# Performance work log

Measured on AMD Instinct MI355X. Metric: run time of the kernel, lower is better.

Reference implementation:

```python
import jax, jax.numpy as jnp
import numpy as np

N = 20000
N_RET = 20000
NEG_SLOPE = 0.2


def _xavier(key, shape):
    fan_in, fan_out = shape[-2], shape[-1]
    limit = float(np.sqrt(6.0 / (fan_in + fan_out)))
    return jax.random.uniform(key, shape, jnp.float32, -limit, limit)


def setup_inputs() -> dict:
    key = jax.random.key(0)
    ks = jax.random.split(key, 24)
    E = 320000
    inp = {
        "emb_u": jax.random.normal(ks[0], (N, 256), jnp.float32),
        "emb_t": jax.random.normal(ks[1], (N, 256), jnp.float32),
        "src_u": jax.random.randint(ks[2], (E,), 0, N, jnp.int32),
        "trg_u": jax.random.randint(ks[3], (E,), 0, N, jnp.int32),
        "src_t": jax.random.randint(ks[4], (E,), 0, N, jnp.int32),
        "trg_t": jax.random.randint(ks[5], (E,), 0, N, jnp.int32),
    }
    # SpGATLayer params per stack (u=user graph, t=tweet graph), 2 layers each.
    # layer0: f_in=256, layer1: f_in = 64*4 = 256 (concat of heads); f_out=64, H=4.
    i = 6
    for side in ("u", "t"):
        for l in range(2):
            inp[f"w_{side}{l}"] = _xavier(ks[i], (4, 256, 64)); i += 1
            inp[f"a_src_{side}{l}"] = _xavier(ks[i], (4, 64, 1))[:, :, 0]; i += 1
            inp[f"a_trg_{side}{l}"] = _xavier(ks[i], (4, 64, 1))[:, :, 0]; i += 1
    inp["fc_w"] = _xavier(ks[i], (128, 16)); i += 1  # [in_features, out_features]
    inp["fc_b"] = jnp.zeros((16,), jnp.float32)
    return inp


def gat_layer(h, w, a_src, a_trg, src, trg):
    # h: [n, f_in], w: [H, f_in, F], a_*: [H, F]
    hp = jnp.einsum("nf,hfo->hno", h, w)                 # [H, n, F]
    attn_src = jnp.einsum("hno,ho->nh", hp, a_src)        # [n, H]
    attn_trg = jnp.einsum("hno,ho->nh", hp, a_trg)        # [n, H]
    e = jax.nn.leaky_relu(attn_src[src] + attn_trg[trg], NEG_SLOPE)  # [E, H]
    exp_e = jnp.exp(e - jnp.max(e))
    denom = jax.ops.segment_sum(exp_e, trg, num_segments=N)[trg] + 1e-16
    attn = (exp_e / denom)[:, :, None]                    # [E, H, 1]
    hp_lift = jnp.transpose(hp, (1, 0, 2))[src]           # [E, H, F]
    return jax.ops.segment_sum(hp_lift * attn, trg, num_segments=N)  # [n, H, F]


def run_stack(h, src, trg, w0, as0, at0, w1, as1, at1):
    x = gat_layer(h, w0, as0, at0, src, trg)
    x = jax.nn.elu(x.reshape(N, -1))                      # [n, H*F]
    x = gat_layer(x, w1, as1, at1, src, trg)
    return x.mean(axis=1)                                 # [n, F]


def reference(emb_u, emb_t, src_u, trg_u, src_t, trg_t,
              w_u0, a_src_u0, a_trg_u0, w_u1, a_src_u1, a_trg_u1,
              w_t0, a_src_t0, a_trg_t0, w_t1, a_src_t1, a_trg_t1,
              fc_w, fc_b):
    out_u = run_stack(emb_u, src_u, trg_u, w_u0, a_src_u0, a_trg_u0, w_u1, a_src_u1, a_trg_u1)
    out_t = run_stack(emb_t, src_t, trg_t, w_t0, a_src_t0, a_trg_t0, w_t1, a_src_t1, a_trg_t1)
    ret = jnp.concatenate([out_u[:N_RET], out_t[:N_RET]], axis=-1)   # [n_ret, 128]
    logits = ret @ fc_w + fc_b                                       # [n_ret, 16]
    return jax.nn.log_softmax(logits, axis=-1)
```

## Files before the change

kernel.cpp:

```cpp
#include <hip/hip_runtime.h>
#include <hip/hip_bf16.h>

#define NEG_SLOPE 0.2f

typedef unsigned short u16;
typedef u16 u16x8 __attribute__((ext_vector_type(8)));
typedef u16 u16x4 __attribute__((ext_vector_type(4)));
typedef short s16x8 __attribute__((ext_vector_type(8)));
typedef float f32x4 __attribute__((ext_vector_type(4)));

__device__ __forceinline__ u16 f2bf(float x) {
    unsigned u = __float_as_uint(x);
    return (u16)((u + 0x7fffu + ((u >> 16) & 1u)) >> 16);
}
__device__ __forceinline__ float bf2f(u16 h) {
    return __uint_as_float(((unsigned)h) << 16);
}

__global__ __launch_bounds__(256) void splitx_k(const float* __restrict__ X,
                                                u16* __restrict__ Xh,
                                                u16* __restrict__ Xl, int total4)
{
    int i = blockIdx.x * 256 + threadIdx.x;
    if (i >= total4) return;
    float4 v = *(const float4*)(X + (size_t)i * 4);
    float f[4] = { v.x, v.y, v.z, v.w };
    u16x4 hi, lo;
    #pragma unroll
    for (int j = 0; j < 4; ++j) {
        u16 h = f2bf(f[j]);
        hi[j] = h;
        lo[j] = f2bf(f[j] - bf2f(h));
    }
    *(u16x4*)(Xh + (size_t)i * 4) = hi;
    *(u16x4*)(Xl + (size_t)i * 4) = lo;
}

__global__ __launch_bounds__(256) void wsplit4_k(
    const float* __restrict__ w0, const float* __restrict__ w1,
    const float* __restrict__ w2, const float* __restrict__ w3,
    u16* __restrict__ Wht, u16* __restrict__ Wlt)
{
    int tid = blockIdx.x * 256 + threadIdx.x;
    int which = tid >> 16;
    int idx = tid & 65535;
    const float* W = (which == 0) ? w0 : (which == 1) ? w1 : (which == 2) ? w2 : w3;
    int f = idx & 63, k = (idx >> 6) & 255, h = idx >> 14;
    float x = W[idx];
    u16 hi = f2bf(x);
    u16 lo = f2bf(x - bf2f(hi));
    int o = (which << 16) + (h * 64 + f) * 256 + k;
    Wht[o] = hi; Wlt[o] = lo;
}

__global__ __launch_bounds__(256) void gemm_mfma_k(
    const u16* __restrict__ Xh, const u16* __restrict__ Xl,
    const u16* __restrict__ Wht, const u16* __restrict__ Wlt,
    const float* __restrict__ a_src, const float* __restrict__ a_trg,
    u16* __restrict__ HPB, float* __restrict__ as_, float* __restrict__ at_,
    int n)
{
    const int row0 = blockIdx.x * 64;
    const int h    = blockIdx.y;
    const int t = threadIdx.x;
    const int l = t & 63;
    const int wc = (t >> 6) & 1;
    const int wr = (t >> 7) & 1;

    __shared__ u16 Ah[64 * 40], Al[64 * 40], Bh[64 * 40], Bl[64 * 40];

    const int sr = t >> 2, sp = t & 3;
    const int arow = (row0 + sr < n) ? (row0 + sr) : (n - 1);
    const u16* gAh = Xh + (size_t)arow * 256 + sp * 8;
    const u16* gAl = Xl + (size_t)arow * 256 + sp * 8;
    const u16* gBh = Wht + (size_t)(h * 64 + sr) * 256 + sp * 8;
    const u16* gBl = Wlt + (size_t)(h * 64 + sr) * 256 + sp * 8;
    const int ldst = sr * 40 + sp * 8;

    const int ra0 = (wr * 32 + (l & 15)) * 40 + (l >> 4) * 8;
    const int ca0 = (wc * 32 + (l & 15)) * 40 + (l >> 4) * 8;

    f32x4 acc00 = {0.f, 0.f, 0.f, 0.f}, acc01 = acc00, acc10 = acc00, acc11 = acc00;

    for (int k0 = 0; k0 < 256; k0 += 32) {
        __syncthreads();
        *(u16x8*)&Ah[ldst] = *(const u16x8*)(gAh + k0);
        *(u16x8*)&Al[ldst] = *(const u16x8*)(gAl + k0);
        *(u16x8*)&Bh[ldst] = *(const u16x8*)(gBh + k0);
        *(u16x8*)&Bl[ldst] = *(const u16x8*)(gBl + k0);
        __syncthreads();

        s16x8 a0h = *(const s16x8*)&Ah[ra0];
        s16x8 a1h = *(const s16x8*)&Ah[ra0 + 640];
        s16x8 a0l = *(const s16x8*)&Al[ra0];
        s16x8 a1l = *(const s16x8*)&Al[ra0 + 640];
        s16x8 b0h = *(const s16x8*)&Bh[ca0];
        s16x8 b1h = *(const s16x8*)&Bh[ca0 + 640];
        s16x8 b0l = *(const s16x8*)&Bl[ca0];
        s16x8 b1l = *(const s16x8*)&Bl[ca0 + 640];

        acc00 = __builtin_amdgcn_mfma_f32_16x16x32_bf16(a0h, b0h, acc00, 0, 0, 0);
        acc01 = __builtin_amdgcn_mfma_f32_16x16x32_bf16(a0h, b1h, acc01, 0, 0, 0);
        acc10 = __builtin_amdgcn_mfma_f32_16x16x32_bf16(a1h, b0h, acc10, 0, 0, 0);
        acc11 = __builtin_amdgcn_mfma_f32_16x16x32_bf16(a1h, b1h, acc11, 0, 0, 0);
        acc00 = __builtin_amdgcn_mfma_f32_16x16x32_bf16(a0h, b0l, acc00, 0, 0, 0);
        acc01 = __builtin_amdgcn_mfma_f32_16x16x32_bf16(a0h, b1l, acc01, 0, 0, 0);
        acc10 = __builtin_amdgcn_mfma_f32_16x16x32_bf16(a1h, b0l, acc10, 0, 0, 0);
        acc11 = __builtin_amdgcn_mfma_f32_16x16x32_bf16(a1h, b1l, acc11, 0, 0, 0);
        acc00 = __builtin_amdgcn_mfma_f32_16x16x32_bf16(a0l, b0h, acc00, 0, 0, 0);
        acc01 = __builtin_amdgcn_mfma_f32_16x16x32_bf16(a0l, b1h, acc01, 0, 0, 0);
        acc10 = __builtin_amdgcn_mfma_f32_16x16x32_bf16(a1l, b0h, acc10, 0, 0, 0);
        acc11 = __builtin_amdgcn_mfma_f32_16x16x32_bf16(a1l, b1h, acc11, 0, 0, 0);
    }

    const int cl = wc * 32 + (l & 15);
    const int rb = row0 + wr * 32 + ((l >> 4) << 2);
    const float pa0 = a_src[h * 64 + cl], pa1 = a_src[h * 64 + cl + 16];
    const float pb0 = a_trg[h * 64 + cl], pb1 = a_trg[h * 64 + cl + 16];

    #pragma unroll
    for (int r = 0; r < 4; ++r) {
        int g0 = rb + r, g1 = rb + 16 + r;
        float s0 = acc00[r] * pa0 + acc01[r] * pa1;
        float t0 = acc00[r] * pb0 + acc01[r] * pb1;
        float s1 = acc10[r] * pa0 + acc11[r] * pa1;
        float t1 = acc10[r] * pb0 + acc11[r] * pb1;
        #pragma unroll
        for (int off = 8; off; off >>= 1) {
            s0 += __shfl_xor(s0, off, 16); t0 += __shfl_xor(t0, off, 16);
            s1 += __shfl_xor(s1, off, 16); t1 += __shfl_xor(t1, off, 16);
        }
        if (g0 < n) {
            HPB[(size_t)g0 * 256 + h * 64 + cl]      = f2bf(acc00[r]);
            HPB[(size_t)g0 * 256 + h * 64 + cl + 16] = f2bf(acc01[r]);
            if ((l & 15) == 0) {
                atomicAdd(&as_[g0 * 4 + h], s0);
                atomicAdd(&at_[g0 * 4 + h], t0);
            }
        }
        if (g1 < n) {
            HPB[(size_t)g1 * 256 + h * 64 + cl]      = f2bf(acc10[r]);
            HPB[(size_t)g1 * 256 + h * 64 + cl + 16] = f2bf(acc11[r]);
            if ((l & 15) == 0) {
                atomicAdd(&as_[g1 * 4 + h], s1);
                atomicAdd(&at_[g1 * 4 + h], t1);
            }
        }
    }
}

__global__ void hist2_k(const int* __restrict__ tu, const int* __restrict__ tt,
                        int* __restrict__ counts, int* __restrict__ ranks,
                        int E, int N)
{
    int e = blockIdx.x * blockDim.x + threadIdx.x;
    if (e < E)          ranks[e] = atomicAdd(&counts[tu[e]], 1);
    else if (e < 2 * E) ranks[e] = atomicAdd(&counts[N + tt[e - E]], 1);
}

__global__ __launch_bounds__(1024) void scan2_k(const int* __restrict__ counts_all,
                                                int* __restrict__ starts_all, int n)
{
    const int T = 1024;
    const int* counts = counts_all + blockIdx.x * n;
    int* starts = starts_all + blockIdx.x * (n + 1);
    int t = threadIdx.x;
    int chunk = (n + T - 1) / T;
    int beg = t * chunk;
    int end = min(beg + chunk, n);
    int sum = 0;
    for (int i = beg; i < end; ++i) sum += counts[i];
    __shared__ int lds[T];
    lds[t] = sum;
    __syncthreads();
    for (int off = 1; off < T; off <<= 1) {
        int v = (t >= off) ? lds[t - off] : 0;
        __syncthreads();
        lds[t] += v;
        __syncthreads();
    }
    int run = lds[t] - sum;
    for (int i = beg; i < end; ++i) { starts[i] = run; run += counts[i]; }
    if (t == T - 1) starts[n] = lds[T - 1];
}

__global__ void scatter2_k(const int* __restrict__ su, const int* __restrict__ st,
                           const int* __restrict__ tu, const int* __restrict__ tt,
                           const int* __restrict__ starts_all,
                           const int* __restrict__ ranks, int* __restrict__ srcs,
                           int E, int N)
{
    int e = blockIdx.x * blockDim.x + threadIdx.x;
    if (e < E) {
        srcs[starts_all[tu[e]] + ranks[e]] = su[e];
    } else if (e < 2 * E) {
        int ee = e - E;
        const int* st1 = starts_all + (N + 1);
        srcs[E + st1[tt[ee]] + ranks[e]] = st[ee];
    }
}

template<int LAYER>
__global__ __launch_bounds__(256) void aggregate_k(
    const u16* __restrict__ HPB, const float* __restrict__ as_,
    const float* __restrict__ at_, const int* __restrict__ starts,
    const int* __restrict__ srcs,
    u16* __restrict__ oh, u16* __restrict__ ol, float* __restrict__ of, int n)
{
    const int w = threadIdx.x >> 6;
    const int l = threadIdx.x & 63;
    const int v = blockIdx.x * 4 + w;
    if (v >= n) return;
    const int h = l >> 4;
    const int s0 = starts[v], s1 = starts[v + 1];
    const float atv = at_[v * 4 + h];
    const size_t lo4 = (size_t)l * 4;

    float4 ac0 = make_float4(0.f, 0.f, 0.f, 0.f), ac1 = ac0, ac2 = ac0, ac3 = ac0;
    float dn0 = 0.f, dn1 = 0.f, dn2 = 0.f, dn3 = 0.f;

    for (int base = s0; base < s1; base += 64) {
        int m = min(64, s1 - base);
        int s_l = (base + l < s1) ? srcs[base + l] : 0;
        int i = 0;
        for (; i + 3 < m; i += 4) {
            int sa = __shfl(s_l, i, 64);
            int sb = __shfl(s_l, i + 1, 64);
            int sc = __shfl(s_l, i + 2, 64);
            int sd = __shfl(s_l, i + 3, 64);
            u16x4 va = *(const u16x4*)(HPB + (size_t)sa * 256 + lo4);
            u16x4 vb = *(const u16x4*)(HPB + (size_t)sb * 256 + lo4);
            u16x4 vc = *(const u16x4*)(HPB + (size_t)sc * 256 + lo4);
            u16x4 vd = *(const u16x4*)(HPB + (size_t)sd * 256 + lo4);
            float ea = as_[sa * 4 + h] + atv;
            float eb = as_[sb * 4 + h] + atv;
            float ec = as_[sc * 4 + h] + atv;
            float ed = as_[sd * 4 + h] + atv;
            ea = (ea > 0.f) ? ea : NEG_SLOPE * ea;
            eb = (eb > 0.f) ? eb : NEG_SLOPE * eb;
            ec = (ec > 0.f) ? ec : NEG_SLOPE * ec;
            ed = (ed > 0.f) ? ed : NEG_SLOPE * ed;
            float pA = expf(ea), pB = expf(eb), pC = expf(ec), pD = expf(ed);
            dn0 += pA; dn1 += pB; dn2 += pC; dn3 += pD;
            ac0.x += pA * bf2f(va[0]); ac0.y += pA * bf2f(va[1]);
            ac0.z += pA * bf2f(va[2]); ac0.w += pA * bf2f(va[3]);
            ac1.x += pB * bf2f(vb[0]); ac1.y += pB * bf2f(vb[1]);
            ac1.z += pB * bf2f(vb[2]); ac1.w += pB * bf2f(vb[3]);
            ac2.x += pC * bf2f(vc[0]); ac2.y += pC * bf2f(vc[1]);
            ac2.z += pC * bf2f(vc[2]); ac2.w += pC * bf2f(vc[3]);
            ac3.x += pD * bf2f(vd[0]); ac3.y += pD * bf2f(vd[1]);
            ac3.z += pD * bf2f(vd[2]); ac3.w += pD * bf2f(vd[3]);
        }
        for (; i < m; ++i) {
            int sa = __shfl(s_l, i, 64);
            u16x4 va = *(const u16x4*)(HPB + (size_t)sa * 256 + lo4);
            float ea = as_[sa * 4 + h] + atv;
            ea = (ea > 0.f) ? ea : NEG_SLOPE * ea;
            float pA = expf(ea);
            dn0 += pA;
            ac0.x += pA * bf2f(va[0]); ac0.y += pA * bf2f(va[1]);
            ac0.z += pA * bf2f(va[2]); ac0.w += pA * bf2f(va[3]);
        }
    }

    float4 acc = make_float4(ac0.x + ac1.x + ac2.x + ac3.x,
                             ac0.y + ac1.y + ac2.y + ac3.y,
                             ac0.z + ac1.z + ac2.z + ac3.z,
                             ac0.w + ac1.w + ac2.w + ac3.w);
    float r = 1.f / (dn0 + dn1 + dn2 + dn3 + 1e-16f);
    acc.x *= r; acc.y *= r; acc.z *= r; acc.w *= r;

    if (LAYER == 0) {
        float f[4] = { acc.x, acc.y, acc.z, acc.w };
        u16x4 hi, lo;
        #pragma unroll
        for (int c = 0; c < 4; ++c) {
            float e = (f[c] > 0.f) ? f[c] : expm1f(f[c]);
            u16 hh = f2bf(e);
            hi[c] = hh;
            lo[c] = f2bf(e - bf2f(hh));
        }
        *(u16x4*)(oh + (size_t)v * 256 + lo4) = hi;
        *(u16x4*)(ol + (size_t)v * 256 + lo4) = lo;
    } else {
        acc.x += __shfl_xor(acc.x, 16, 64); acc.y += __shfl_xor(acc.y, 16, 64);
        acc.z += __shfl_xor(acc.z, 16, 64); acc.w += __shfl_xor(acc.w, 16, 64);
        acc.x += __shfl_xor(acc.x, 32, 64); acc.y += __shfl_xor(acc.y, 32, 64);
        acc.z += __shfl_xor(acc.z, 32, 64); acc.w += __shfl_xor(acc.w, 32, 64);
        if (l < 16) {
            acc.x *= 0.25f; acc.y *= 0.25f; acc.z *= 0.25f; acc.w *= 0.25f;
            *(float4*)(of + (size_t)v * 64 + l * 4) = acc;
        }
    }
}

__global__ __launch_bounds__(256) void final_k(
    const float* __restrict__ out_u, const float* __restrict__ out_t,
    const float* __restrict__ fcw, const float* __restrict__ fcb,
    float* __restrict__ out, int nret)
{
    int gid = blockIdx.x * blockDim.x + threadIdx.x;
    int nn = gid >> 4;
    int j  = gid & 15;
    if (nn >= nret) return;
    const float* ru = out_u + (size_t)nn * 64;
    const float* rt = out_t + (size_t)nn * 64;
    float acc = fcb[j];
    #pragma unroll 8
    for (int k = 0; k < 64; ++k) acc += ru[k] * fcw[k * 16 + j];
    #pragma unroll 8
    for (int k = 0; k < 64; ++k) acc += rt[k] * fcw[(64 + k) * 16 + j];

    float m = acc;
    for (int off = 8; off; off >>= 1) m = fmaxf(m, __shfl_xor(m, off, 16));
    float ex = expf(acc - m);
    float s = ex;
    for (int off = 8; off; off >>= 1) s += __shfl_xor(s, off, 16);
    out[(size_t)nn * 16 + j] = acc - m - logf(s);
}

extern "C" void kernel_launch(void* const* d_in, const int* in_sizes, int n_in,
                              void* d_out, int out_size, void* d_ws, size_t ws_size,
                              hipStream_t stream)
{
    const int N = in_sizes[0] / 256;
    const int E = in_sizes[2];
    const int NRET = out_size / 16;

    const float* emb[2]  = { (const float*)d_in[0], (const float*)d_in[1] };
    const int*   srcI[2] = { (const int*)d_in[2], (const int*)d_in[4] };
    const int*   trgI[2] = { (const int*)d_in[3], (const int*)d_in[5] };
    const float* fcw = (const float*)d_in[18];
    const float* fcb = (const float*)d_in[19];

    char* p = (char*)d_ws;
    u16* hpb = (u16*)p;   p += (size_t)N * 256 * 2;
    u16* xh  = (u16*)p;   p += (size_t)N * 256 * 2;
    u16* xl  = (u16*)p;   p += (size_t)N * 256 * 2;
    u16* wht = (u16*)p;   p += (size_t)4 * 65536 * 2;
    u16* wlt = (u16*)p;   p += (size_t)4 * 65536 * 2;
    float* asat = (float*)p; p += (size_t)N * 32 * 4;
    float* out_s[2];
    out_s[0] = (float*)p; p += (size_t)N * 64 * 4;
    out_s[1] = (float*)p; p += (size_t)N * 64 * 4;
    int* starts2 = (int*)p; p += (size_t)2 * (N + 1) * 4;
    int* counts2 = (int*)p; p += (size_t)2 * N * 4;
    int* ranks2  = (int*)p; p += (size_t)2 * E * 4;
    int* srcs2   = (int*)p; p += (size_t)2 * E * 4;

    const int E2B = (2 * E + 255) / 256;
    const dim3 gemm_grid((N + 63) / 64, 4);
    const int split_blocks = (N * 64 + 255) / 256;
    const int agg_grid = (N + 3) / 4;

    hipMemsetAsync(asat, 0, (size_t)N * 32 * 4, stream);
    hipMemsetAsync(counts2, 0, (size_t)2 * N * 4, stream);

    hist2_k<<<E2B, 256, 0, stream>>>(trgI[0], trgI[1], counts2, ranks2, E, N);
    scan2_k<<<2, 1024, 0, stream>>>(counts2, starts2, N);
    scatter2_k<<<E2B, 256, 0, stream>>>(srcI[0], srcI[1], trgI[0], trgI[1],
                                        starts2, ranks2, srcs2, E, N);

    wsplit4_k<<<1024, 256, 0, stream>>>(
        (const float*)d_in[6], (const float*)d_in[9],
        (const float*)d_in[12], (const float*)d_in[15], wht, wlt);

    for (int side = 0; side < 2; ++side) {
        const int* starts = starts2 + side * (N + 1);
        const int* srcs   = srcs2 + side * E;

        splitx_k<<<split_blocks, 256, 0, stream>>>(emb[side], xh, xl, N * 64);

        for (int layer = 0; layer < 2; ++layer) {
            const int which = side * 2 + layer;
            const float* asl = (const float*)d_in[6 + side * 6 + layer * 3 + 1];
            const float* atl = (const float*)d_in[6 + side * 6 + layer * 3 + 2];
            float* as_ = asat + (size_t)which * N * 8;
            float* at_ = as_ + (size_t)N * 4;

            gemm_mfma_k<<<gemm_grid, 256, 0, stream>>>(
                xh, xl, wht + (size_t)which * 65536, wlt + (size_t)which * 65536,
                asl, atl, hpb, as_, at_, N);

            if (layer == 0)
                aggregate_k<0><<<agg_grid, 256, 0, stream>>>(
                    hpb, as_, at_, starts, srcs, xh, xl, nullptr, N);
            else
                aggregate_k<1><<<agg_grid, 256, 0, stream>>>(
                    hpb, as_, at_, starts, srcs, nullptr, nullptr, out_s[side], N);
        }
    }

    final_k<<<(NRET * 16 + 255) / 256, 256, 0, stream>>>(out_s[0], out_s[1], fcw, fcb,
                                                         (float*)d_out, NRET);
}
```

Measured before the change: 453.1 us.

## Batch both graph stacks per launch and widen GEMM tile to all heads

Runs the user and tweet stacks together by adding a side dimension to the grid of the split, GEMM and aggregate kernels, which halves the number of launches and doubles the parallelism available to each. The GEMM now computes all four heads per block (64 rows by 256 columns, one wave per head), so the A tile is reused across heads. Because each wave owns a full head, the attention dot products can be written directly instead of atomically added, and the asat memset is removed. In exchange each block holds a much larger LDS footprint for B, uses more accumulator registers, and workspace buffers double in size, which may lower occupancy.

```diff
diff --git a/kernel.cpp b/kernel.cpp
--- a/kernel.cpp
+++ b/kernel.cpp
@@ -17,12 +17,15 @@
     return __uint_as_float(((unsigned)h) << 16);
 }
 
-__global__ __launch_bounds__(256) void splitx_k(const float* __restrict__ X,
-                                                u16* __restrict__ Xh,
-                                                u16* __restrict__ Xl, int total4)
+__global__ __launch_bounds__(256) void splitx_k(
+    const float* __restrict__ x0, const float* __restrict__ x1,
+    u16* __restrict__ Xh, u16* __restrict__ Xl, int per_side4)
 {
     int i = blockIdx.x * 256 + threadIdx.x;
-    if (i >= total4) return;
+    if (i >= per_side4) return;
+    int side = blockIdx.y;
+    const float* X = side ? x1 : x0;
+    size_t o = (size_t)side * per_side4 * 4 + (size_t)i * 4;
     float4 v = *(const float4*)(X + (size_t)i * 4);
     float f[4] = { v.x, v.y, v.z, v.w };
     u16x4 hi, lo;
@@ -32,8 +35,8 @@
         hi[j] = h;
         lo[j] = f2bf(f[j] - bf2f(h));
     }
-    *(u16x4*)(Xh + (size_t)i * 4) = hi;
-    *(u16x4*)(Xl + (size_t)i * 4) = lo;
+    *(u16x4*)(Xh + o) = hi;
+    *(u16x4*)(Xl + o) = lo;
 }
 
 __global__ __launch_bounds__(256) void wsplit4_k(
@@ -54,96 +57,114 @@
 }
 
 __global__ __launch_bounds__(256) void gemm_mfma_k(
-    const u16* __restrict__ Xh, const u16* __restrict__ Xl,
+    const u16* __restrict__ xh_all, const u16* __restrict__ xl_all,
     const u16* __restrict__ Wht, const u16* __restrict__ Wlt,
-    const float* __restrict__ a_src, const float* __restrict__ a_trg,
-    u16* __restrict__ HPB, float* __restrict__ as_, float* __restrict__ at_,
-    int n)
-{
+    const float* __restrict__ au_s, const float* __restrict__ au_t,
+    const float* __restrict__ at_s, const float* __restrict__ at_t,
+    u16* __restrict__ hpb_all,
+    float* __restrict__ asat,
+    int layer, int n)
+{
+    const int side = blockIdx.y;
     const int row0 = blockIdx.x * 64;
-    const int h    = blockIdx.y;
     const int t = threadIdx.x;
     const int l = t & 63;
-    const int wc = (t >> 6) & 1;
-    const int wr = (t >> 7) & 1;
-
-    __shared__ u16 Ah[64 * 40], Al[64 * 40], Bh[64 * 40], Bl[64 * 40];
+    const int h = t >> 6;
+    const int which = side * 2 + layer;
+
+    const u16* Xh = xh_all + (size_t)side * n * 256;
+    const u16* Xl = xl_all + (size_t)side * n * 256;
+    const u16* Wh = Wht + ((size_t)which << 16);
+    const u16* Wl = Wlt + ((size_t)which << 16);
+    const float* a_src = (side ? at_s : au_s) + h * 64;
+    const float* a_trg = (side ? at_t : au_t) + h * 64;
+    u16* HPB = hpb_all + (size_t)side * n * 256;
+    float* as_ = asat + (size_t)which * n * 8;
+    float* at_ = as_ + (size_t)n * 4;
+
+    __shared__ u16 Ah[64 * 40], Al[64 * 40], Bh[256 * 40], Bl[256 * 40];
 
     const int sr = t >> 2, sp = t & 3;
     const int arow = (row0 + sr < n) ? (row0 + sr) : (n - 1);
     const u16* gAh = Xh + (size_t)arow * 256 + sp * 8;
     const u16* gAl = Xl + (size_t)arow * 256 + sp * 8;
-    const u16* gBh = Wht + (size_t)(h * 64 + sr) * 256 + sp * 8;
-    const u16* gBl = Wlt + (size_t)(h * 64 + sr) * 256 + sp * 8;
-    const int ldst = sr * 40 + sp * 8;
-
-    const int ra0 = (wr * 32 + (l & 15)) * 40 + (l >> 4) * 8;
-    const int ca0 = (wc * 32 + (l & 15)) * 40 + (l >> 4) * 8;
-
-    f32x4 acc00 = {0.f, 0.f, 0.f, 0.f}, acc01 = acc00, acc10 = acc00, acc11 = acc00;
+    const int lda = sr * 40 + sp * 8;
+
+    const int fb = l & 15;
+    const int kg = l >> 4;
+    int ra[4], cb[4];
+    #pragma unroll
+    for (int r = 0; r < 4; ++r) ra[r] = (r * 16 + fb) * 40 + kg * 8;
+    #pragma unroll
+    for (int c = 0; c < 4; ++c) cb[c] = (h * 64 + c * 16 + fb) * 40 + kg * 8;
+
+    f32x4 acc[4][4];
+    #pragma unroll
+    for (int r = 0; r < 4; ++r)
+        #pragma unroll
+        for (int c = 0; c < 4; ++c) acc[r][c] = f32x4{0.f, 0.f, 0.f, 0.f};
 
     for (int k0 = 0; k0 < 256; k0 += 32) {
         __syncthreads();
-        *(u16x8*)&Ah[ldst] = *(const u16x8*)(gAh + k0);
-        *(u16x8*)&Al[ldst] = *(const u16x8*)(gAl + k0);
-        *(u16x8*)&Bh[ldst] = *(const u16x8*)(gBh + k0);
-        *(u16x8*)&Bl[ldst] = *(const u16x8*)(gBl + k0);
+        *(u16x8*)&Ah[lda] = *(const u16x8*)(gAh + k0);
+        *(u16x8*)&Al[lda] = *(const u16x8*)(gAl + k0);
+        #pragma unroll
+        for (int i = 0; i < 4; ++i) {
+            int j = t + i * 256;
+            int col = j >> 2, cp = j & 3;
+            int ofs = col * 40 + cp * 8;
+            *(u16x8*)&Bh[ofs] = *(const u16x8*)(Wh + (size_t)col * 256 + k0 + cp * 8);
+            *(u16x8*)&Bl[ofs] = *(const u16x8*)(Wl + (size_t)col * 256 + k0 + cp * 8);
+        }
         __syncthreads();
 
-        s16x8 a0h = *(const s16x8*)&Ah[ra0];
-        s16x8 a1h = *(const s16x8*)&Ah[ra0 + 640];
-        s16x8 a0l = *(const s16x8*)&Al[ra0];
-        s16x8 a1l = *(const s16x8*)&Al[ra0 + 640];
-        s16x8 b0h = *(const s16x8*)&Bh[ca0];
-        s16x8 b1h = *(const s16x8*)&Bh[ca0 + 640];
-        s16x8 b0l = *(const s16x8*)&Bl[ca0];
-        s16x8 b1l = *(const s16x8*)&Bl[ca0 + 640];
-
-        acc00 = __builtin_amdgcn_mfma_f32_16x16x32_bf16(a0h, b0h, acc00, 0, 0, 0);
-        acc01 = __builtin_amdgcn_mfma_f32_16x16x32_bf16(a0h, b1h, acc01, 0, 0, 0);
-        acc10 = __builtin_amdgcn_mfma_f32_16x16x32_bf16(a1h, b0h, acc10, 0, 0, 0);
-        acc11 = __builtin_amdgcn_mfma_f32_16x16x32_bf16(a1h, b1h, acc11, 0, 0, 0);
-        acc00 = __builtin_amdgcn_mfma_f32_16x16x32_bf16(a0h, b0l, acc00, 0, 0, 0);
-        acc01 = __builtin_amdgcn_mfma_f32_16x16x32_bf16(a0h, b1l, acc01, 0, 0, 0);
-        acc10 = __builtin_amdgcn_mfma_f32_16x16x32_bf16(a1h, b0l, acc10, 0, 0, 0);
-        acc11 = __builtin_amdgcn_mfma_f32_16x16x32_bf16(a1h, b1l, acc11, 0, 0, 0);
-        acc00 = __builtin_amdgcn_mfma_f32_16x16x32_bf16(a0l, b0h, acc00, 0, 0, 0);
-        acc01 = __builtin_amdgcn_mfma_f32_16x16x32_bf16(a0l, b1h, acc01, 0, 0, 0);
-        acc10 = __builtin_amdgcn_mfma_f32_16x16x32_bf16(a1l, b0h, acc10, 0, 0, 0);
-        acc11 = __builtin_amdgcn_mfma_f32_16x16x32_bf16(a1l, b1h, acc11, 0, 0, 0);
-    }
-
-    const int cl = wc * 32 + (l & 15);
-    const int rb = row0 + wr * 32 + ((l >> 4) << 2);
-    const float pa0 = a_src[h * 64 + cl], pa1 = a_src[h * 64 + cl + 16];
-    const float pb0 = a_trg[h * 64 + cl], pb1 = a_trg[h * 64 + cl + 16];
+        s16x8 bh[4], bl[4];
+        #pragma unroll
+        for (int c = 0; c < 4; ++c) {
+            bh[c] = *(const s16x8*)&Bh[cb[c]];
+            bl[c] = *(const s16x8*)&Bl[cb[c]];
+        }
+        #pragma unroll
+        for (int r = 0; r < 4; ++r) {
+            s16x8 ah = *(const s16x8*)&Ah[ra[r]];
+            s16x8 al = *(const s16x8*)&Al[ra[r]];
+            #pragma unroll
+            for (int c = 0; c < 4; ++c) {
+                acc[r][c] = __builtin_amdgcn_mfma_f32_16x16x32_bf16(ah, bh[c], acc[r][c], 0, 0, 0);
+                acc[r][c] = __builtin_amdgcn_mfma_f32_16x16x32_bf16(ah, bl[c], acc[r][c], 0, 0, 0);
+                acc[r][c] = __builtin_amdgcn_mfma_f32_16x16x32_bf16(al, bh[c], acc[r][c], 0, 0, 0);
+            }
+        }
+    }
+
+    float pav[4], pbv[4];
+    #pragma unroll
+    for (int c = 0; c < 4; ++c) { pav[c] = a_src[c * 16 + fb]; pbv[c] = a_trg[c * 16 + fb]; }
 
     #pragma unroll
     for (int r = 0; r < 4; ++r) {
-        int g0 = rb + r, g1 = rb + 16 + r;
-        float s0 = acc00[r] * pa0 + acc01[r] * pa1;
-        float t0 = acc00[r] * pb0 + acc01[r] * pb1;
-        float s1 = acc10[r] * pa0 + acc11[r] * pa1;
-        float t1 = acc10[r] * pb0 + acc11[r] * pb1;
-        #pragma unroll
-        for (int off = 8; off; off >>= 1) {
-            s0 += __shfl_xor(s0, off, 16); t0 += __shfl_xor(t0, off, 16);
-            s1 += __shfl_xor(s1, off, 16); t1 += __shfl_xor(t1, off, 16);
-        }
-        if (g0 < n) {
-            HPB[(size_t)g0 * 256 + h * 64 + cl]      = f2bf(acc00[r]);
-            HPB[(size_t)g0 * 256 + h * 64 + cl + 16] = f2bf(acc01[r]);
-            if ((l & 15) == 0) {
-                atomicAdd(&as_[g0 * 4 + h], s0);
-                atomicAdd(&at_[g0 * 4 + h], t0);
+        #pragma unroll
+        for (int q = 0; q < 4; ++q) {
+            int grow = row0 + r * 16 + kg * 4 + q;
+            float s = 0.f, u = 0.f;
+            if (grow < n) {
+                u16* hrow = HPB + (size_t)grow * 256 + h * 64 + fb;
+                #pragma unroll
+                for (int c = 0; c < 4; ++c) {
+                    float v = acc[r][c][q];
+                    s += v * pav[c];
+                    u += v * pbv[c];
+                    hrow[c * 16] = f2bf(v);
+                }
             }
-        }
-        if (g1 < n) {
-            HPB[(size_t)g1 * 256 + h * 64 + cl]      = f2bf(acc10[r]);
-            HPB[(size_t)g1 * 256 + h * 64 + cl + 16] = f2bf(acc11[r]);
-            if ((l & 15) == 0) {
-                atomicAdd(&as_[g1 * 4 + h], s1);
-                atomicAdd(&at_[g1 * 4 + h], t1);
+            #pragma unroll
+            for (int off = 8; off; off >>= 1) {
+                s += __shfl_xor(s, off, 16);
+                u += __shfl_xor(u, off, 16);
+            }
+            if (grow < n && fb == 0) {
+                as_[grow * 4 + h] = s;
+                at_[grow * 4 + h] = u;
             }
         }
     }
@@ -202,16 +223,25 @@
 
 template<int LAYER>
 __global__ __launch_bounds__(256) void aggregate_k(
-    const u16* __restrict__ HPB, const float* __restrict__ as_,
-    const float* __restrict__ at_, const int* __restrict__ starts,
-    const int* __restrict__ srcs,
-    u16* __restrict__ oh, u16* __restrict__ ol, float* __restrict__ of, int n)
-{
+    const u16* __restrict__ hpb_all, const float* __restrict__ asat,
+    const int* __restrict__ starts2, const int* __restrict__ srcs2,
+    u16* __restrict__ oh_all, u16* __restrict__ ol_all,
+    float* __restrict__ of_all, int n, int E)
+{
+    const int side = blockIdx.y;
     const int w = threadIdx.x >> 6;
     const int l = threadIdx.x & 63;
     const int v = blockIdx.x * 4 + w;
     if (v >= n) return;
     const int h = l >> 4;
+    const int which = side * 2 + LAYER;
+
+    const u16* HPB = hpb_all + (size_t)side * n * 256;
+    const float* as_ = asat + (size_t)which * n * 8;
+    const float* at_ = as_ + (size_t)n * 4;
+    const int* starts = starts2 + side * (n + 1);
+    const int* srcs = srcs2 + (size_t)side * E;
+
     const int s0 = starts[v], s1 = starts[v + 1];
     const float atv = at_[v * 4 + h];
     const size_t lo4 = (size_t)l * 4;
@@ -271,6 +301,8 @@
     acc.x *= r; acc.y *= r; acc.z *= r; acc.w *= r;
 
     if (LAYER == 0) {
+        u16* oh = oh_all + (size_t)side * n * 256;
+        u16* ol = ol_all + (size_t)side * n * 256;
         float f[4] = { acc.x, acc.y, acc.z, acc.w };
         u16x4 hi, lo;
         #pragma unroll
@@ -283,6 +315,7 @@
         *(u16x4*)(oh + (size_t)v * 256 + lo4) = hi;
         *(u16x4*)(ol + (size_t)v * 256 + lo4) = lo;
     } else {
+        float* of = of_all + (size_t)side * n * 64;
         acc.x += __shfl_xor(acc.x, 16, 64); acc.y += __shfl_xor(acc.y, 16, 64);
         acc.z += __shfl_xor(acc.z, 16, 64); acc.w += __shfl_xor(acc.w, 16, 64);
         acc.x += __shfl_xor(acc.x, 32, 64); acc.y += __shfl_xor(acc.y, 32, 64);
@@ -334,26 +367,23 @@
     const float* fcb = (const float*)d_in[19];
 
     char* p = (char*)d_ws;
-    u16* hpb = (u16*)p;   p += (size_t)N * 256 * 2;
-    u16* xh  = (u16*)p;   p += (size_t)N * 256 * 2;
-    u16* xl  = (u16*)p;   p += (size_t)N * 256 * 2;
-    u16* wht = (u16*)p;   p += (size_t)4 * 65536 * 2;
-    u16* wlt = (u16*)p;   p += (size_t)4 * 65536 * 2;
-    float* asat = (float*)p; p += (size_t)N * 32 * 4;
-    float* out_s[2];
-    out_s[0] = (float*)p; p += (size_t)N * 64 * 4;
-    out_s[1] = (float*)p; p += (size_t)N * 64 * 4;
+    u16* hpb  = (u16*)p;    p += (size_t)2 * N * 256 * 2;
+    u16* xh   = (u16*)p;    p += (size_t)2 * N * 256 * 2;
+    u16* xl   = (u16*)p;    p += (size_t)2 * N * 256 * 2;
+    u16* wht  = (u16*)p;    p += (size_t)4 * 65536 * 2;
+    u16* wlt  = (u16*)p;    p += (size_t)4 * 65536 * 2;
+    float* asat = (float*)p; p += (size_t)4 * N * 8 * 4;
+    float* outs = (float*)p; p += (size_t)2 * N * 64 * 4;
     int* starts2 = (int*)p; p += (size_t)2 * (N + 1) * 4;
     int* counts2 = (int*)p; p += (size_t)2 * N * 4;
     int* ranks2  = (int*)p; p += (size_t)2 * E * 4;
     int* srcs2   = (int*)p; p += (size_t)2 * E * 4;
 
     const int E2B = (2 * E + 255) / 256;
-    const dim3 gemm_grid((N + 63) / 64, 4);
-    const int split_blocks = (N * 64 + 255) / 256;
-    const int agg_grid = (N + 3) / 4;
-
-    hipMemsetAsync(asat, 0, (size_t)N * 32 * 4, stream);
+    const dim3 gemm_grid((N + 63) / 64, 2);
+    const dim3 split_grid((N * 64 + 255) / 256, 2);
+    const dim3 agg_grid((N + 3) / 4, 2);
+
     hipMemsetAsync(counts2, 0, (size_t)2 * N * 4, stream);
 
     hist2_k<<<E2B, 256, 0, stream>>>(trgI[0], trgI[1], counts2, ranks2, E, N);
@@ -365,32 +395,25 @@
         (const float*)d_in[6], (const float*)d_in[9],
         (const float*)d_in[12], (const float*)d_in[15], wht, wlt);
 
-    for (int side = 0; side < 2; ++side) {
-        const int* starts = starts2 + side * (N + 1);
-        const int* srcs   = srcs2 + side * E;
-
-        splitx_k<<<split_blocks, 256, 0, stream>>>(emb[side], xh, xl, N * 64);
-
-        for (int layer = 0; layer < 2; ++layer) {
-            const int which = side * 2 + layer;
-            const float* asl = (const float*)d_in[6 + side * 6 + layer * 3 + 1];
-            const float* atl = (const float*)d_in[6 + side * 6 + layer * 3 + 2];
-            float* as_ = asat + (size_t)which * N * 8;
-            float* at_ = as_ + (size_t)N * 4;
-
-            gemm_mfma_k<<<gemm_grid, 256, 0, stream>>>(
-                xh, xl, wht + (size_t)which * 65536, wlt + (size_t)which * 65536,
-                asl, atl, hpb, as_, at_, N);
-
-            if (layer == 0)
-                aggregate_k<0><<<agg_grid, 256, 0, stream>>>(
-                    hpb, as_, at_, starts, srcs, xh, xl, nullptr, N);
-            else
-                aggregate_k<1><<<agg_grid, 256, 0, stream>>>(
-                    hpb, as_, at_, starts, srcs, nullptr, nullptr, out_s[side], N);
-        }
-    }
-
-    final_k<<<(NRET * 16 + 255) / 256, 256, 0, stream>>>(out_s[0], out_s[1], fcw, fcb,
-                                                         (float*)d_out, NRET);
-}
+    splitx_k<<<split_grid, 256, 0, stream>>>(emb[0], emb[1], xh, xl, N * 64);
+
+    for (int layer = 0; layer < 2; ++layer) {
+        const float* au_s = (const float*)d_in[6 + 0 * 6 + layer * 3 + 1];
+        const float* au_t = (const float*)d_in[6 + 0 * 6 + layer * 3 + 2];
+        const float* at_s = (const float*)d_in[6 + 1 * 6 + layer * 3 + 1];
+        const float* at_t = (const float*)d_in[6 + 1 * 6 + layer * 3 + 2];
+
+        gemm_mfma_k<<<gemm_grid, 256, 0, stream>>>(
+            xh, xl, wht, wlt, au_s, au_t, at_s, at_t, hpb, asat, layer, N);
+
+        if (layer == 0)
+            aggregate_k<0><<<agg_grid, 256, 0, stream>>>(
+                hpb, asat, starts2, srcs2, xh, xl, nullptr, N, E);
+        else
+            aggregate_k<1><<<agg_grid, 256, 0, stream>>>(
+                hpb, asat, starts2, srcs2, nullptr, nullptr, outs, N, E);
+    }
+
+    final_k<<<(NRET * 16 + 255) / 256, 256, 0, stream>>>(
+        outs, outs + (size_t)N * 64, fcw, fcb, (float*)d_out, NRET);
+}
```

New measurement: 384.4 us. 1.18x faster.
